# Kernel optimization log

Measured on AMD Instinct MI355X. Metric: run time of the kernel, lower is better.

Reference implementation:

```python
import jax, jax.numpy as jnp
import numpy as np

NEG_INF = -1e30  # stand-in for -inf, avoids NaN under masked rows edge cases


def setup_inputs() -> dict:
    key = jax.random.key(0)
    ks = jax.random.split(key, 6)
    H, N, F_IN, HD, F_OUT = 8, 4096, 512, 64, 512
    X = jax.random.normal(ks[0], (H, N, F_IN), dtype=jnp.float32)
    mask = jax.random.randint(ks[1], (H, N, N), 0, 2, dtype=jnp.int32)
    s = 1.0 / np.sqrt(F_IN)
    W_Q = jax.random.normal(ks[2], (H, HD, F_IN), dtype=jnp.float32) * s
    W_K = jax.random.normal(ks[3], (H, HD, F_IN), dtype=jnp.float32) * s
    W_V = jax.random.normal(ks[4], (H, HD, F_IN), dtype=jnp.float32) * s
    W_O = jax.random.normal(ks[5], (F_OUT, H * HD), dtype=jnp.float32) * (1.0 / np.sqrt(H * HD))
    return {"X": X, "mask": mask, "W_Q": W_Q, "W_K": W_K, "W_V": W_V, "W_O": W_O}


def reference(X, mask, W_Q, W_K, W_V, W_O):
    # X: [H, N, F_in]; W_{Q,K,V}: [H, head_dim, F_in] (torch Linear layout: [out,in])
    Q = jnp.einsum('hnf,hdf->hnd', X, W_Q)
    K = jnp.einsum('hnf,hdf->hnd', X, W_K)
    V = jnp.einsum('hnf,hdf->hnd', X, W_V)
    head_dim = K.shape[-1]
    E = jnp.einsum('hnd,hmd->hnm', Q, K) / jnp.sqrt(jnp.float32(head_dim))  # [H,N,N]
    E = jnp.where(mask == 0, jnp.float32(NEG_INF), E)
    A = jax.nn.softmax(E, axis=-1)
    Hout = jnp.einsum('hnm,hmd->hnd', A, V)  # [H, N, head_dim]
    # concat heads along feature dim -> [N, H*head_dim]
    Hcat = jnp.transpose(Hout, (1, 0, 2)).reshape(Hout.shape[1], -1)
    # dropout is identity in eval mode
    return Hcat @ W_O.T  # [N, fan_out]
```

## Files before the change

### kernel.cpp

```cpp
#include <hip/hip_runtime.h>

typedef __bf16 bf16x8 __attribute__((ext_vector_type(8)));
typedef float f32x4 __attribute__((ext_vector_type(4)));
typedef int i32x4 __attribute__((ext_vector_type(4)));

#define MFMA(a, b, c) __builtin_amdgcn_mfma_f32_16x16x32_bf16((a), (b), (c), 0, 0, 0)
#define GLOAD_LDS(g, l) __builtin_amdgcn_global_load_lds( \
    (const __attribute__((address_space(1))) void*)(g),   \
    (__attribute__((address_space(3))) void*)(l), 16, 0, 0)

constexpr int HEADS = 8, SEQ = 4096, FIN = 512, HD = 64, FOUT = 512;
constexpr float QSCALE = 0.18033688011112042f;

__device__ inline bf16x8 cvt8(const float* __restrict__ p) {
    f32x4 a = *(const f32x4*)p;
    f32x4 b = *(const f32x4*)(p + 4);
    bf16x8 r;
    r[0] = (__bf16)a[0]; r[1] = (__bf16)a[1]; r[2] = (__bf16)a[2]; r[3] = (__bf16)a[3];
    r[4] = (__bf16)b[0]; r[5] = (__bf16)b[1]; r[6] = (__bf16)b[2]; r[7] = (__bf16)b[3];
    return r;
}

__global__ __launch_bounds__(256) void qkv_kernel(
    const float* __restrict__ X, const float* __restrict__ Wq,
    const float* __restrict__ Wk, const float* __restrict__ Wv,
    __bf16* __restrict__ Q, __bf16* __restrict__ K, __bf16* __restrict__ Vt)
{
    const int h = blockIdx.y;
    const int tid = threadIdx.x;
    const int w = tid >> 6, lane = tid & 63;
    const int quad = lane >> 4, l16 = lane & 15;
    const int m = blockIdx.x * 64 + w * 16 + l16;

    const float* xrow = X + ((size_t)h * SEQ + m) * FIN + quad * 8;
    const float* wqh = Wq + (size_t)h * HD * FIN + quad * 8;
    const float* wkh = Wk + (size_t)h * HD * FIN + quad * 8;
    const float* wvh = Wv + (size_t)h * HD * FIN + quad * 8;

    const f32x4 vzero = {0.f, 0.f, 0.f, 0.f};
    f32x4 accQ[4], accK[4], accV[4];
#pragma unroll
    for (int t = 0; t < 4; ++t) { accQ[t] = vzero; accK[t] = vzero; accV[t] = vzero; }

    for (int f0 = 0; f0 < FIN; f0 += 32) {
        bf16x8 a = cvt8(xrow + f0);
#pragma unroll
        for (int t = 0; t < 4; ++t) {
            const int wrow = (t * 16 + l16) * FIN + f0;
            bf16x8 bq = cvt8(wqh + wrow);
            bf16x8 bk = cvt8(wkh + wrow);
            bf16x8 bv = cvt8(wvh + wrow);
            accQ[t] = MFMA(a, bq, accQ[t]);
            accK[t] = MFMA(a, bk, accK[t]);
            accV[t] = MFMA(a, bv, accV[t]);
        }
    }

    const int row0 = blockIdx.x * 64 + w * 16 + quad * 4;
#pragma unroll
    for (int t = 0; t < 4; ++t) {
        const int d = t * 16 + l16;
#pragma unroll
        for (int r = 0; r < 4; ++r) {
            const int n = row0 + r;
            Q[((size_t)h * SEQ + n) * HD + d] = (__bf16)(accQ[t][r] * QSCALE);
            K[((size_t)h * SEQ + n) * HD + d] = (__bf16)accK[t][r];
            Vt[((size_t)h * HD + d) * SEQ + n] = (__bf16)accV[t][r];
        }
    }
}

__global__ __launch_bounds__(256) void attn_kernel(
    const __bf16* __restrict__ Q, const __bf16* __restrict__ K,
    const __bf16* __restrict__ Vt, const int* __restrict__ mask,
    __bf16* __restrict__ Hcat)
{
    __shared__ __align__(16) unsigned char lds[32768 + 4 * 2048];

    const int bid = blockIdx.x;
    const int h = bid & 7;
    const int q0b = (bid >> 3) * 64;
    const int tid = threadIdx.x;
    const int w = tid >> 6, lane = tid & 63;
    const int quad = lane >> 4, l16 = lane & 15;
    const int q0 = q0b + w * 16;
    const int e7 = l16 & 7;

    __bf16* PT = (__bf16*)(lds + 32768) + w * 1024;

    const __bf16* Qh = Q + (size_t)h * SEQ * HD;
    const __bf16* Kh = K + (size_t)h * SEQ * HD;
    const __bf16* Vh = Vt + (size_t)h * HD * SEQ;
    const int* mrow = mask + ((size_t)h * SEQ + q0 + l16) * SEQ + quad * 4;

    auto stage = [&](int n0, int b) {
        unsigned char* bK = lds + b * 8192;
        unsigned char* bV = lds + 16384 + b * 8192;
#pragma unroll
        for (int c = 0; c < 2; ++c) {
            const int s = c * 256 + w * 64 + lane;
            const int row = s >> 3;
            const int cq = (s & 7) ^ (row & 7);
            GLOAD_LDS(Kh + (size_t)(n0 + row) * HD + cq * 8, bK + (c * 256 + w * 64) * 16);
            GLOAD_LDS(Vh + (size_t)row * SEQ + n0 + cq * 8, bV + (c * 256 + w * 64) * 16);
        }
    };
    auto loadM = [&](int n0, i32x4* mv) {
#pragma unroll
        for (int t = 0; t < 4; ++t) mv[t] = *(const i32x4*)(mrow + n0 + t * 16);
    };

    bf16x8 qa0 = *(const bf16x8*)(Qh + (size_t)(q0 + l16) * HD + quad * 8);
    bf16x8 qa1 = *(const bf16x8*)(Qh + (size_t)(q0 + l16) * HD + 32 + quad * 8);

    const f32x4 vzero = {0.f, 0.f, 0.f, 0.f};
    f32x4 O[4];
    float ls0 = 0.f, ls1 = 0.f, ls2 = 0.f, ls3 = 0.f;
#pragma unroll
    for (int t = 0; t < 4; ++t) O[t] = vzero;

    i32x4 mA[4], mB[4];
    stage(0, 0);
    loadM(0, mA);
    __syncthreads();

    auto tile = [&](int i, const i32x4* mc, i32x4* mn) {
        const int n0 = i * 64;
        const int cur = i & 1;
        if (i + 1 < SEQ / 64) {
            stage(n0 + 64, cur ^ 1);
            loadM(n0 + 64, mn);
        }
        const __bf16* cK = (const __bf16*)(lds + cur * 8192);
        const __bf16* cV = (const __bf16*)(lds + 16384 + cur * 8192);

        f32x4 St[4];
        __builtin_amdgcn_s_setprio(1);
#pragma unroll
        for (int t = 0; t < 4; ++t) {
            const int kr = t * 16 + l16;
            bf16x8 kb0 = *(const bf16x8*)(cK + kr * 64 + ((quad ^ (kr & 7)) * 8));
            bf16x8 kb1 = *(const bf16x8*)(cK + kr * 64 + (((quad + 4) ^ (kr & 7)) * 8));
            St[t] = MFMA(kb0, qa0, vzero);
            St[t] = MFMA(kb1, qa1, St[t]);
        }
        __builtin_amdgcn_s_setprio(0);

#pragma unroll
        for (int t = 0; t < 4; ++t) {
            union { unsigned long long u; __bf16 hh[4]; } pk;
            float psub0 = 0.f, psub1 = 0.f;
#pragma unroll
            for (int r = 0; r < 4; ++r) {
                float p = __builtin_amdgcn_exp2f(St[t][r]);
                p = mc[t][r] ? p : 0.f;
                if (r & 1) psub1 += p; else psub0 += p;
                pk.hh[r] = (__bf16)p;
            }
            if (t == 0) ls0 += psub0 + psub1;
            else if (t == 1) ls1 += psub0 + psub1;
            else if (t == 2) ls2 += psub0 + psub1;
            else ls3 += psub0 + psub1;
            const int c = t * 2 + (quad >> 1);
            *(unsigned long long*)(PT + l16 * 64 + ((c ^ e7) * 8) + (quad & 1) * 4) = pk.u;
        }

        bf16x8 pa0 = *(const bf16x8*)(PT + l16 * 64 + ((quad ^ e7) * 8));
        bf16x8 pa1 = *(const bf16x8*)(PT + l16 * 64 + (((quad + 4) ^ e7) * 8));
        __builtin_amdgcn_s_setprio(1);
#pragma unroll
        for (int t = 0; t < 4; ++t) {
            const int dr = t * 16 + l16;
            bf16x8 vb0 = *(const bf16x8*)(cV + dr * 64 + ((quad ^ (dr & 7)) * 8));
            bf16x8 vb1 = *(const bf16x8*)(cV + dr * 64 + (((quad + 4) ^ (dr & 7)) * 8));
            O[t] = MFMA(pa0, vb0, O[t]);
            O[t] = MFMA(pa1, vb1, O[t]);
        }
        __builtin_amdgcn_s_setprio(0);
        __syncthreads();
    };

    for (int i = 0; i < SEQ / 64; i += 2) {
        tile(i, mA, mB);
        tile(i + 1, mB, mA);
    }

    float lsum = (ls0 + ls1) + (ls2 + ls3);
    lsum += __shfl_xor(lsum, 16, 64);
    lsum += __shfl_xor(lsum, 32, 64);
    float inv[4];
#pragma unroll
    for (int r = 0; r < 4; ++r) {
        float Lr = __shfl(lsum, quad * 4 + r, 64);
        inv[r] = Lr > 0.f ? 1.0f / Lr : 0.f;
    }

#pragma unroll
    for (int r = 0; r < 4; ++r) {
        const int n = q0 + quad * 4 + r;
#pragma unroll
        for (int t = 0; t < 4; ++t)
            Hcat[(size_t)n * FOUT + h * HD + t * 16 + l16] = (__bf16)(O[t][r] * inv[r]);
    }
}

__global__ __launch_bounds__(256) void out_kernel(
    const __bf16* __restrict__ Hcat, const float* __restrict__ Wo,
    float* __restrict__ out)
{
    const int tid = threadIdx.x;
    const int w = tid >> 6, lane = tid & 63;
    const int quad = lane >> 4, l16 = lane & 15;
    const int n0 = blockIdx.x * 64 + w * 16;
    const int o0 = blockIdx.y * 64;

    const f32x4 vzero = {0.f, 0.f, 0.f, 0.f};
    f32x4 acc[4];
#pragma unroll
    for (int t = 0; t < 4; ++t) acc[t] = vzero;

    for (int k0 = 0; k0 < FOUT; k0 += 32) {
        bf16x8 a = *(const bf16x8*)(Hcat + (size_t)(n0 + l16) * FOUT + k0 + quad * 8);
#pragma unroll
        for (int t = 0; t < 4; ++t) {
            bf16x8 b = cvt8(Wo + (size_t)(o0 + t * 16 + l16) * FOUT + k0 + quad * 8);
            acc[t] = MFMA(a, b, acc[t]);
        }
    }
#pragma unroll
    for (int t = 0; t < 4; ++t)
#pragma unroll
        for (int r = 0; r < 4; ++r)
            out[(size_t)(n0 + quad * 4 + r) * FOUT + o0 + t * 16 + l16] = acc[t][r];
}

extern "C" void kernel_launch(void* const* d_in, const int* in_sizes, int n_in,
                              void* d_out, int out_size, void* d_ws, size_t ws_size,
                              hipStream_t stream) {
    const float* X    = (const float*)d_in[0];
    const int*   mask = (const int*)d_in[1];
    const float* Wq   = (const float*)d_in[2];
    const float* Wk   = (const float*)d_in[3];
    const float* Wv   = (const float*)d_in[4];
    const float* Wo   = (const float*)d_in[5];
    float* out = (float*)d_out;

    __bf16* Q    = (__bf16*)d_ws;
    __bf16* K    = Q + (size_t)HEADS * SEQ * HD;
    __bf16* Vt   = K + (size_t)HEADS * SEQ * HD;
    __bf16* Hcat = Vt + (size_t)HEADS * HD * SEQ;

    qkv_kernel<<<dim3(SEQ / 64, HEADS), 256, 0, stream>>>(X, Wq, Wk, Wv, Q, K, Vt);
    attn_kernel<<<(SEQ / 64) * HEADS, 256, 0, stream>>>(Q, K, Vt, mask, Hcat);
    out_kernel<<<dim3(SEQ / 64, FOUT / 64), 256, 0, stream>>>(Hcat, Wo, out);
}
```

Measured before the change: 889.5 us.

## Pack int32 mask into 64-bit bitmasks in a pre-pass before attention

Adds a pack kernel that reads the int32 attention mask once and writes one 64-bit ballot word per 64 keys per query row. The attention kernel then loads a single u64 per tile instead of four i32x4 vectors and tests bits, which cuts mask traffic and register use inside the main loop. The cost is an extra launch that still streams the full 512MB mask, plus a small workspace region for the packed words. Since the mask must be read in full either way, any gain depends on the attention loop having been limited by mask loads.

```diff
diff --git a/kernel.cpp b/kernel.cpp
--- a/kernel.cpp
+++ b/kernel.cpp
@@ -21,6 +21,20 @@
     return r;
 }
 
+__global__ __launch_bounds__(256) void pack_kernel(
+    const int* __restrict__ mask, unsigned long long* __restrict__ pmask)
+{
+    const int w = threadIdx.x >> 6, lane = threadIdx.x & 63;
+    const size_t row = (size_t)blockIdx.x * 4 + w;
+    const int* mr = mask + row * SEQ;
+    unsigned long long* pr = pmask + row * (SEQ / 64);
+    for (int tw = 0; tw < SEQ / 64; ++tw) {
+        int m = mr[tw * 64 + lane];
+        unsigned long long b = __ballot(m != 0);
+        if (lane == 0) pr[tw] = b;
+    }
+}
+
 __global__ __launch_bounds__(256) void qkv_kernel(
     const float* __restrict__ X, const float* __restrict__ Wq,
     const float* __restrict__ Wk, const float* __restrict__ Wv,
@@ -72,7 +86,7 @@
 
 __global__ __launch_bounds__(256) void attn_kernel(
     const __bf16* __restrict__ Q, const __bf16* __restrict__ K,
-    const __bf16* __restrict__ Vt, const int* __restrict__ mask,
+    const __bf16* __restrict__ Vt, const unsigned long long* __restrict__ pmask,
     __bf16* __restrict__ Hcat)
 {
     __shared__ __align__(16) unsigned char lds[32768 + 4 * 2048];
@@ -85,13 +99,14 @@
     const int quad = lane >> 4, l16 = lane & 15;
     const int q0 = q0b + w * 16;
     const int e7 = l16 & 7;
+    const int qsh = quad * 4;
 
     __bf16* PT = (__bf16*)(lds + 32768) + w * 1024;
 
     const __bf16* Qh = Q + (size_t)h * SEQ * HD;
     const __bf16* Kh = K + (size_t)h * SEQ * HD;
     const __bf16* Vh = Vt + (size_t)h * HD * SEQ;
-    const int* mrow = mask + ((size_t)h * SEQ + q0 + l16) * SEQ + quad * 4;
+    const unsigned long long* pmr = pmask + ((size_t)h * SEQ + q0 + l16) * (SEQ / 64);
 
     auto stage = [&](int n0, int b) {
         unsigned char* bK = lds + b * 8192;
@@ -105,10 +120,6 @@
             GLOAD_LDS(Vh + (size_t)row * SEQ + n0 + cq * 8, bV + (c * 256 + w * 64) * 16);
         }
     };
-    auto loadM = [&](int n0, i32x4* mv) {
-#pragma unroll
-        for (int t = 0; t < 4; ++t) mv[t] = *(const i32x4*)(mrow + n0 + t * 16);
-    };
 
     bf16x8 qa0 = *(const bf16x8*)(Qh + (size_t)(q0 + l16) * HD + quad * 8);
     bf16x8 qa1 = *(const bf16x8*)(Qh + (size_t)(q0 + l16) * HD + 32 + quad * 8);
@@ -119,17 +130,17 @@
 #pragma unroll
     for (int t = 0; t < 4; ++t) O[t] = vzero;
 
-    i32x4 mA[4], mB[4];
+    unsigned long long mA, mB;
     stage(0, 0);
-    loadM(0, mA);
+    mA = pmr[0];
     __syncthreads();
 
-    auto tile = [&](int i, const i32x4* mc, i32x4* mn) {
+    auto tile = [&](int i, unsigned long long mc, unsigned long long* mn) {
         const int n0 = i * 64;
         const int cur = i & 1;
         if (i + 1 < SEQ / 64) {
             stage(n0 + 64, cur ^ 1);
-            loadM(n0 + 64, mn);
+            *mn = pmr[i + 1];
         }
         const __bf16* cK = (const __bf16*)(lds + cur * 8192);
         const __bf16* cV = (const __bf16*)(lds + 16384 + cur * 8192);
@@ -146,14 +157,16 @@
         }
         __builtin_amdgcn_s_setprio(0);
 
-#pragma unroll
-        for (int t = 0; t < 4; ++t) {
+        const unsigned mlo = (unsigned)mc, mhi = (unsigned)(mc >> 32);
+#pragma unroll
+        for (int t = 0; t < 4; ++t) {
+            const unsigned ms = (((t & 2) ? mhi : mlo) >> ((t & 1) * 16)) >> qsh;
             union { unsigned long long u; __bf16 hh[4]; } pk;
             float psub0 = 0.f, psub1 = 0.f;
 #pragma unroll
             for (int r = 0; r < 4; ++r) {
                 float p = __builtin_amdgcn_exp2f(St[t][r]);
-                p = mc[t][r] ? p : 0.f;
+                p = (ms & (1u << r)) ? p : 0.f;
                 if (r & 1) psub1 += p; else psub0 += p;
                 pk.hh[r] = (__bf16)p;
             }
@@ -181,8 +194,8 @@
     };
 
     for (int i = 0; i < SEQ / 64; i += 2) {
-        tile(i, mA, mB);
-        tile(i + 1, mB, mA);
+        tile(i, mA, &mB);
+        tile(i + 1, mB, &mA);
     }
 
     float lsum = (ls0 + ls1) + (ls2 + ls3);
@@ -249,8 +262,10 @@
     __bf16* K    = Q + (size_t)HEADS * SEQ * HD;
     __bf16* Vt   = K + (size_t)HEADS * SEQ * HD;
     __bf16* Hcat = Vt + (size_t)HEADS * HD * SEQ;
-
+    unsigned long long* pmask = (unsigned long long*)(Hcat + (size_t)SEQ * FOUT);
+
+    pack_kernel<<<HEADS * SEQ / 4, 256, 0, stream>>>(mask, pmask);
     qkv_kernel<<<dim3(SEQ / 64, HEADS), 256, 0, stream>>>(X, Wq, Wk, Wv, Q, K, Vt);
-    attn_kernel<<<(SEQ / 64) * HEADS, 256, 0, stream>>>(Q, K, Vt, mask, Hcat);
+    attn_kernel<<<(SEQ / 64) * HEADS, 256, 0, stream>>>(Q, K, Vt, pmask, Hcat);
     out_kernel<<<dim3(SEQ / 64, FOUT / 64), 256, 0, stream>>>(Hcat, Wo, out);
 }
```

After: 976.5 us. 1.1x slower.

## Load K and V tiles directly from global memory instead of LDS staging

Applied to the files above, without the earlier changes.

Removes the double-buffered global_load_lds staging of K and V tiles and the per-tile block barrier. Each wave now reads its K and V fragments straight from global memory, relying on L1/L2 caching since all four waves of a block read the same tiles. This frees LDS, which could raise occupancy, and removes the synchronisation. The cost is redundant global loads per wave and no explicit prefetch, so load latency now sits directly in front of the MFMAs.

```diff
diff --git a/kernel.cpp b/kernel.cpp
--- a/kernel.cpp
+++ b/kernel.cpp
@@ -5,9 +5,6 @@
 typedef int i32x4 __attribute__((ext_vector_type(4)));
 
 #define MFMA(a, b, c) __builtin_amdgcn_mfma_f32_16x16x32_bf16((a), (b), (c), 0, 0, 0)
-#define GLOAD_LDS(g, l) __builtin_amdgcn_global_load_lds( \
-    (const __attribute__((address_space(1))) void*)(g),   \
-    (__attribute__((address_space(3))) void*)(l), 16, 0, 0)
 
 constexpr int HEADS = 8, SEQ = 4096, FIN = 512, HD = 64, FOUT = 512;
 constexpr float QSCALE = 0.18033688011112042f;
@@ -75,7 +72,7 @@
     const __bf16* __restrict__ Vt, const int* __restrict__ mask,
     __bf16* __restrict__ Hcat)
 {
-    __shared__ __align__(16) unsigned char lds[32768 + 4 * 2048];
+    __shared__ __align__(16) __bf16 PT_lds[4 * 1024];
 
     const int bid = blockIdx.x;
     const int h = bid & 7;
@@ -86,25 +83,13 @@
     const int q0 = q0b + w * 16;
     const int e7 = l16 & 7;
 
-    __bf16* PT = (__bf16*)(lds + 32768) + w * 1024;
+    __bf16* PT = PT_lds + w * 1024;
 
     const __bf16* Qh = Q + (size_t)h * SEQ * HD;
     const __bf16* Kh = K + (size_t)h * SEQ * HD;
     const __bf16* Vh = Vt + (size_t)h * HD * SEQ;
     const int* mrow = mask + ((size_t)h * SEQ + q0 + l16) * SEQ + quad * 4;
 
-    auto stage = [&](int n0, int b) {
-        unsigned char* bK = lds + b * 8192;
-        unsigned char* bV = lds + 16384 + b * 8192;
-#pragma unroll
-        for (int c = 0; c < 2; ++c) {
-            const int s = c * 256 + w * 64 + lane;
-            const int row = s >> 3;
-            const int cq = (s & 7) ^ (row & 7);
-            GLOAD_LDS(Kh + (size_t)(n0 + row) * HD + cq * 8, bK + (c * 256 + w * 64) * 16);
-            GLOAD_LDS(Vh + (size_t)row * SEQ + n0 + cq * 8, bV + (c * 256 + w * 64) * 16);
-        }
-    };
     auto loadM = [&](int n0, i32x4* mv) {
 #pragma unroll
         for (int t = 0; t < 4; ++t) mv[t] = *(const i32x4*)(mrow + n0 + t * 16);
@@ -120,27 +105,19 @@
     for (int t = 0; t < 4; ++t) O[t] = vzero;
 
     i32x4 mA[4], mB[4];
-    stage(0, 0);
     loadM(0, mA);
-    __syncthreads();
 
     auto tile = [&](int i, const i32x4* mc, i32x4* mn) {
         const int n0 = i * 64;
-        const int cur = i & 1;
-        if (i + 1 < SEQ / 64) {
-            stage(n0 + 64, cur ^ 1);
-            loadM(n0 + 64, mn);
-        }
-        const __bf16* cK = (const __bf16*)(lds + cur * 8192);
-        const __bf16* cV = (const __bf16*)(lds + 16384 + cur * 8192);
+        if (i + 1 < SEQ / 64) loadM(n0 + 64, mn);
 
         f32x4 St[4];
         __builtin_amdgcn_s_setprio(1);
 #pragma unroll
         for (int t = 0; t < 4; ++t) {
-            const int kr = t * 16 + l16;
-            bf16x8 kb0 = *(const bf16x8*)(cK + kr * 64 + ((quad ^ (kr & 7)) * 8));
-            bf16x8 kb1 = *(const bf16x8*)(cK + kr * 64 + (((quad + 4) ^ (kr & 7)) * 8));
+            const __bf16* krow = Kh + (size_t)(n0 + t * 16 + l16) * HD;
+            bf16x8 kb0 = *(const bf16x8*)(krow + quad * 8);
+            bf16x8 kb1 = *(const bf16x8*)(krow + 32 + quad * 8);
             St[t] = MFMA(kb0, qa0, vzero);
             St[t] = MFMA(kb1, qa1, St[t]);
         }
@@ -170,14 +147,13 @@
         __builtin_amdgcn_s_setprio(1);
 #pragma unroll
         for (int t = 0; t < 4; ++t) {
-            const int dr = t * 16 + l16;
-            bf16x8 vb0 = *(const bf16x8*)(cV + dr * 64 + ((quad ^ (dr & 7)) * 8));
-            bf16x8 vb1 = *(const bf16x8*)(cV + dr * 64 + (((quad + 4) ^ (dr & 7)) * 8));
+            const __bf16* vrow = Vh + (size_t)(t * 16 + l16) * SEQ + n0;
+            bf16x8 vb0 = *(const bf16x8*)(vrow + quad * 8);
+            bf16x8 vb1 = *(const bf16x8*)(vrow + 32 + quad * 8);
             O[t] = MFMA(pa0, vb0, O[t]);
             O[t] = MFMA(pa1, vb1, O[t]);
         }
         __builtin_amdgcn_s_setprio(0);
-        __syncthreads();
     };
 
     for (int i = 0; i < SEQ / 64; i += 2) {
```

New measurement: 1.036 ms. 16.4% more time.

## Use 32x32 MFMA with split-K warps in attention and pre-convert weights to bf16

Applied to the files above, without the earlier changes.

The attention kernel now uses 32x32x16 MFMAs. Each wave handles 32 queries and half of each 64-key tile, and the P operand is rebuilt through cross-lane shuffles instead of an LDS round trip. The two key-halves' partial outputs and row sums are reduced through LDS at the end, and stores are vectorized. A separate kernel converts the weight matrices to bf16 once per call, so the projection kernels load bf16 directly instead of converting fp32 in their inner loops. This adds a launch and a final LDS reduction, and the attention loop remains bound by streaming the int32 mask.

```diff
diff --git a/kernel.cpp b/kernel.cpp
--- a/kernel.cpp
+++ b/kernel.cpp
@@ -2,9 +2,11 @@
 
 typedef __bf16 bf16x8 __attribute__((ext_vector_type(8)));
 typedef float f32x4 __attribute__((ext_vector_type(4)));
+typedef float f32x16 __attribute__((ext_vector_type(16)));
 typedef int i32x4 __attribute__((ext_vector_type(4)));
 
-#define MFMA(a, b, c) __builtin_amdgcn_mfma_f32_16x16x32_bf16((a), (b), (c), 0, 0, 0)
+#define MFMA16(a, b, c) __builtin_amdgcn_mfma_f32_16x16x32_bf16((a), (b), (c), 0, 0, 0)
+#define MFMA32(a, b, c) __builtin_amdgcn_mfma_f32_32x32x16_bf16((a), (b), (c), 0, 0, 0)
 #define GLOAD_LDS(g, l) __builtin_amdgcn_global_load_lds( \
     (const __attribute__((address_space(1))) void*)(g),   \
     (__attribute__((address_space(3))) void*)(l), 16, 0, 0)
@@ -21,9 +23,28 @@
     return r;
 }
 
+__device__ inline unsigned pack2(float a, float b) {
+    union { unsigned u; __bf16 h[2]; } r;
+    r.h[0] = (__bf16)a; r.h[1] = (__bf16)b;
+    return r.u;
+}
+
+__global__ __launch_bounds__(256) void wconv_kernel(
+    const float* __restrict__ Wq, const float* __restrict__ Wk,
+    const float* __restrict__ Wv, const float* __restrict__ Wo,
+    __bf16* __restrict__ oq, __bf16* __restrict__ ok,
+    __bf16* __restrict__ ov, __bf16* __restrict__ oo)
+{
+    const int which = blockIdx.y;
+    const float* s = which == 0 ? Wq : which == 1 ? Wk : which == 2 ? Wv : Wo;
+    __bf16* d = which == 0 ? oq : which == 1 ? ok : which == 2 ? ov : oo;
+    const size_t i = ((size_t)blockIdx.x * 256 + threadIdx.x) * 8;
+    *(bf16x8*)(d + i) = cvt8(s + i);
+}
+
 __global__ __launch_bounds__(256) void qkv_kernel(
-    const float* __restrict__ X, const float* __restrict__ Wq,
-    const float* __restrict__ Wk, const float* __restrict__ Wv,
+    const float* __restrict__ X, const __bf16* __restrict__ Wq,
+    const __bf16* __restrict__ Wk, const __bf16* __restrict__ Wv,
     __bf16* __restrict__ Q, __bf16* __restrict__ K, __bf16* __restrict__ Vt)
 {
     const int h = blockIdx.y;
@@ -33,9 +54,9 @@
     const int m = blockIdx.x * 64 + w * 16 + l16;
 
     const float* xrow = X + ((size_t)h * SEQ + m) * FIN + quad * 8;
-    const float* wqh = Wq + (size_t)h * HD * FIN + quad * 8;
-    const float* wkh = Wk + (size_t)h * HD * FIN + quad * 8;
-    const float* wvh = Wv + (size_t)h * HD * FIN + quad * 8;
+    const __bf16* wqh = Wq + (size_t)h * HD * FIN + quad * 8;
+    const __bf16* wkh = Wk + (size_t)h * HD * FIN + quad * 8;
+    const __bf16* wvh = Wv + (size_t)h * HD * FIN + quad * 8;
 
     const f32x4 vzero = {0.f, 0.f, 0.f, 0.f};
     f32x4 accQ[4], accK[4], accV[4];
@@ -47,12 +68,12 @@
 #pragma unroll
         for (int t = 0; t < 4; ++t) {
             const int wrow = (t * 16 + l16) * FIN + f0;
-            bf16x8 bq = cvt8(wqh + wrow);
-            bf16x8 bk = cvt8(wkh + wrow);
-            bf16x8 bv = cvt8(wvh + wrow);
-            accQ[t] = MFMA(a, bq, accQ[t]);
-            accK[t] = MFMA(a, bk, accK[t]);
-            accV[t] = MFMA(a, bv, accV[t]);
+            bf16x8 bq = *(const bf16x8*)(wqh + wrow);
+            bf16x8 bk = *(const bf16x8*)(wkh + wrow);
+            bf16x8 bv = *(const bf16x8*)(wvh + wrow);
+            accQ[t] = MFMA16(a, bq, accQ[t]);
+            accK[t] = MFMA16(a, bk, accK[t]);
+            accV[t] = MFMA16(a, bv, accV[t]);
         }
     }
 
@@ -75,23 +96,22 @@
     const __bf16* __restrict__ Vt, const int* __restrict__ mask,
     __bf16* __restrict__ Hcat)
 {
-    __shared__ __align__(16) unsigned char lds[32768 + 4 * 2048];
+    __shared__ __align__(16) unsigned char lds[4 * 32 * 68 * 4 + 4 * 32 * 4];
 
     const int bid = blockIdx.x;
     const int h = bid & 7;
     const int q0b = (bid >> 3) * 64;
     const int tid = threadIdx.x;
     const int w = tid >> 6, lane = tid & 63;
-    const int quad = lane >> 4, l16 = lane & 15;
-    const int q0 = q0b + w * 16;
-    const int e7 = l16 & 7;
-
-    __bf16* PT = (__bf16*)(lds + 32768) + w * 1024;
+    const int qh = w >> 1;
+    const int kh = w & 1;
+    const int l32 = lane & 31;
+    const int hi = lane >> 5;
 
     const __bf16* Qh = Q + (size_t)h * SEQ * HD;
     const __bf16* Kh = K + (size_t)h * SEQ * HD;
     const __bf16* Vh = Vt + (size_t)h * HD * SEQ;
-    const int* mrow = mask + ((size_t)h * SEQ + q0 + l16) * SEQ + quad * 4;
+    const int* mrow = mask + ((size_t)h * SEQ + q0b + qh * 32 + l32) * SEQ + kh * 32 + hi * 4;
 
     auto stage = [&](int n0, int b) {
         unsigned char* bK = lds + b * 8192;
@@ -107,22 +127,24 @@
     };
     auto loadM = [&](int n0, i32x4* mv) {
 #pragma unroll
-        for (int t = 0; t < 4; ++t) mv[t] = *(const i32x4*)(mrow + n0 + t * 16);
+        for (int c = 0; c < 4; ++c) mv[c] = *(const i32x4*)(mrow + n0 + c * 8);
     };
 
-    bf16x8 qa0 = *(const bf16x8*)(Qh + (size_t)(q0 + l16) * HD + quad * 8);
-    bf16x8 qa1 = *(const bf16x8*)(Qh + (size_t)(q0 + l16) * HD + 32 + quad * 8);
-
-    const f32x4 vzero = {0.f, 0.f, 0.f, 0.f};
-    f32x4 O[4];
+    bf16x8 qb[4];
+#pragma unroll
+    for (int s = 0; s < 4; ++s)
+        qb[s] = *(const bf16x8*)(Qh + (size_t)(q0b + qh * 32 + l32) * HD + s * 16 + hi * 8);
+
+    f32x16 O0 = {}, O1 = {};
     float ls0 = 0.f, ls1 = 0.f, ls2 = 0.f, ls3 = 0.f;
-#pragma unroll
-    for (int t = 0; t < 4; ++t) O[t] = vzero;
 
     i32x4 mA[4], mB[4];
     stage(0, 0);
     loadM(0, mA);
     __syncthreads();
+
+    const int krow = kh * 32 + l32;
+    const int ksw = krow & 7;
 
     auto tile = [&](int i, const i32x4* mc, i32x4* mn) {
         const int n0 = i * 64;
@@ -134,47 +156,59 @@
         const __bf16* cK = (const __bf16*)(lds + cur * 8192);
         const __bf16* cV = (const __bf16*)(lds + 16384 + cur * 8192);
 
-        f32x4 St[4];
+        f32x16 St = {};
         __builtin_amdgcn_s_setprio(1);
 #pragma unroll
-        for (int t = 0; t < 4; ++t) {
-            const int kr = t * 16 + l16;
-            bf16x8 kb0 = *(const bf16x8*)(cK + kr * 64 + ((quad ^ (kr & 7)) * 8));
-            bf16x8 kb1 = *(const bf16x8*)(cK + kr * 64 + (((quad + 4) ^ (kr & 7)) * 8));
-            St[t] = MFMA(kb0, qa0, vzero);
-            St[t] = MFMA(kb1, qa1, St[t]);
+        for (int s = 0; s < 4; ++s) {
+            bf16x8 ka = *(const bf16x8*)(cK + krow * 64 + (((2 * s + hi) ^ ksw) * 8));
+            St = MFMA32(ka, qb[s], St);
         }
         __builtin_amdgcn_s_setprio(0);
 
-#pragma unroll
-        for (int t = 0; t < 4; ++t) {
-            union { unsigned long long u; __bf16 hh[4]; } pk;
-            float psub0 = 0.f, psub1 = 0.f;
-#pragma unroll
-            for (int r = 0; r < 4; ++r) {
-                float p = __builtin_amdgcn_exp2f(St[t][r]);
-                p = mc[t][r] ? p : 0.f;
-                if (r & 1) psub1 += p; else psub0 += p;
-                pk.hh[r] = (__bf16)p;
+        float p[16];
+#pragma unroll
+        for (int c = 0; c < 4; ++c) {
+            float a0 = 0.f, a1 = 0.f;
+#pragma unroll
+            for (int j = 0; j < 4; ++j) {
+                float e = __builtin_amdgcn_exp2f(St[c * 4 + j]);
+                e = mc[c][j] ? e : 0.f;
+                if (j & 1) a1 += e; else a0 += e;
+                p[c * 4 + j] = e;
             }
-            if (t == 0) ls0 += psub0 + psub1;
-            else if (t == 1) ls1 += psub0 + psub1;
-            else if (t == 2) ls2 += psub0 + psub1;
-            else ls3 += psub0 + psub1;
-            const int c = t * 2 + (quad >> 1);
-            *(unsigned long long*)(PT + l16 * 64 + ((c ^ e7) * 8) + (quad & 1) * 4) = pk.u;
-        }
-
-        bf16x8 pa0 = *(const bf16x8*)(PT + l16 * 64 + ((quad ^ e7) * 8));
-        bf16x8 pa1 = *(const bf16x8*)(PT + l16 * 64 + (((quad + 4) ^ e7) * 8));
+            if (c == 0) ls0 += a0 + a1;
+            else if (c == 1) ls1 += a0 + a1;
+            else if (c == 2) ls2 += a0 + a1;
+            else ls3 += a0 + a1;
+        }
+
+        bf16x8 pa[2];
+#pragma unroll
+        for (int sp = 0; sp < 2; ++sp) {
+            unsigned u0 = pack2(p[sp * 8 + 0], p[sp * 8 + 1]);
+            unsigned u1 = pack2(p[sp * 8 + 2], p[sp * 8 + 3]);
+            unsigned u2 = pack2(p[sp * 8 + 4], p[sp * 8 + 5]);
+            unsigned u3 = pack2(p[sp * 8 + 6], p[sp * 8 + 7]);
+            unsigned s0 = (unsigned)__shfl_xor((int)u0, 32, 64);
+            unsigned s1 = (unsigned)__shfl_xor((int)u1, 32, 64);
+            unsigned s2 = (unsigned)__shfl_xor((int)u2, 32, 64);
+            unsigned s3 = (unsigned)__shfl_xor((int)u3, 32, 64);
+            union { unsigned u[4]; bf16x8 v; } A;
+            A.u[0] = hi ? s2 : u0;
+            A.u[1] = hi ? s3 : u1;
+            A.u[2] = hi ? u2 : s0;
+            A.u[3] = hi ? u3 : s1;
+            pa[sp] = A.v;
+        }
+
         __builtin_amdgcn_s_setprio(1);
 #pragma unroll
-        for (int t = 0; t < 4; ++t) {
-            const int dr = t * 16 + l16;
-            bf16x8 vb0 = *(const bf16x8*)(cV + dr * 64 + ((quad ^ (dr & 7)) * 8));
-            bf16x8 vb1 = *(const bf16x8*)(cV + dr * 64 + (((quad + 4) ^ (dr & 7)) * 8));
-            O[t] = MFMA(pa0, vb0, O[t]);
-            O[t] = MFMA(pa1, vb1, O[t]);
+        for (int sp = 0; sp < 2; ++sp) {
+            const int g = kh * 4 + 2 * sp + hi;
+            bf16x8 vb0 = *(const bf16x8*)(cV + l32 * 64 + ((g ^ (l32 & 7)) * 8));
+            bf16x8 vb1 = *(const bf16x8*)(cV + (32 + l32) * 64 + ((g ^ ((32 + l32) & 7)) * 8));
+            O0 = MFMA32(pa[sp], vb0, O0);
+            O1 = MFMA32(pa[sp], vb1, O1);
         }
         __builtin_amdgcn_s_setprio(0);
         __syncthreads();
@@ -185,27 +219,45 @@
         tile(i + 1, mB, mA);
     }
 
+    float* Of = (float*)lds;
+    float* Lf = (float*)lds + 4 * 32 * 68;
     float lsum = (ls0 + ls1) + (ls2 + ls3);
-    lsum += __shfl_xor(lsum, 16, 64);
     lsum += __shfl_xor(lsum, 32, 64);
-    float inv[4];
-#pragma unroll
-    for (int r = 0; r < 4; ++r) {
-        float Lr = __shfl(lsum, quad * 4 + r, 64);
-        inv[r] = Lr > 0.f ? 1.0f / Lr : 0.f;
-    }
-
-#pragma unroll
-    for (int r = 0; r < 4; ++r) {
-        const int n = q0 + quad * 4 + r;
-#pragma unroll
-        for (int t = 0; t < 4; ++t)
-            Hcat[(size_t)n * FOUT + h * HD + t * 16 + l16] = (__bf16)(O[t][r] * inv[r]);
-    }
+    float* myO = Of + w * (32 * 68);
+#pragma unroll
+    for (int r = 0; r < 16; ++r) {
+        const int qr = (r & 3) + 8 * (r >> 2) + 4 * hi;
+        myO[qr * 68 + l32] = O0[r];
+        myO[qr * 68 + 32 + l32] = O1[r];
+    }
+    if (lane < 32) Lf[w * 32 + lane] = lsum;
+    __syncthreads();
+
+    const int q = tid >> 2, hd0 = (tid & 3) * 16;
+    const int qg = q >> 5, q32 = q & 31;
+    const float l = Lf[qg * 64 + q32] + Lf[qg * 64 + 32 + q32];
+    const float inv = l > 0.f ? 1.0f / l : 0.f;
+    float acc[16];
+#pragma unroll
+    for (int v = 0; v < 4; ++v) {
+        f32x4 a = *(const f32x4*)(Of + (2 * qg) * (32 * 68) + q32 * 68 + hd0 + v * 4);
+        f32x4 b = *(const f32x4*)(Of + (2 * qg + 1) * (32 * 68) + q32 * 68 + hd0 + v * 4);
+#pragma unroll
+        for (int j = 0; j < 4; ++j) acc[v * 4 + j] = a[j] + b[j];
+    }
+    bf16x8 o0, o1;
+#pragma unroll
+    for (int j = 0; j < 8; ++j) {
+        o0[j] = (__bf16)(acc[j] * inv);
+        o1[j] = (__bf16)(acc[8 + j] * inv);
+    }
+    __bf16* dst = Hcat + (size_t)(q0b + q) * FOUT + h * HD + hd0;
+    *(bf16x8*)dst = o0;
+    *(bf16x8*)(dst + 8) = o1;
 }
 
 __global__ __launch_bounds__(256) void out_kernel(
-    const __bf16* __restrict__ Hcat, const float* __restrict__ Wo,
+    const __bf16* __restrict__ Hcat, const __bf16* __restrict__ Wo,
     float* __restrict__ out)
 {
     const int tid = threadIdx.x;
@@ -223,8 +275,8 @@
         bf16x8 a = *(const bf16x8*)(Hcat + (size_t)(n0 + l16) * FOUT + k0 + quad * 8);
 #pragma unroll
         for (int t = 0; t < 4; ++t) {
-            bf16x8 b = cvt8(Wo + (size_t)(o0 + t * 16 + l16) * FOUT + k0 + quad * 8);
-            acc[t] = MFMA(a, b, acc[t]);
+            bf16x8 b = *(const bf16x8*)(Wo + (size_t)(o0 + t * 16 + l16) * FOUT + k0 + quad * 8);
+            acc[t] = MFMA16(a, b, acc[t]);
         }
     }
 #pragma unroll
@@ -249,8 +301,13 @@
     __bf16* K    = Q + (size_t)HEADS * SEQ * HD;
     __bf16* Vt   = K + (size_t)HEADS * SEQ * HD;
     __bf16* Hcat = Vt + (size_t)HEADS * HD * SEQ;
-
-    qkv_kernel<<<dim3(SEQ / 64, HEADS), 256, 0, stream>>>(X, Wq, Wk, Wv, Q, K, Vt);
+    __bf16* Wqb  = Hcat + (size_t)SEQ * FOUT;
+    __bf16* Wkb  = Wqb + (size_t)HEADS * HD * FIN;
+    __bf16* Wvb  = Wkb + (size_t)HEADS * HD * FIN;
+    __bf16* Wob  = Wvb + (size_t)HEADS * HD * FIN;
+
+    wconv_kernel<<<dim3(128, 4), 256, 0, stream>>>(Wq, Wk, Wv, Wo, Wqb, Wkb, Wvb, Wob);
+    qkv_kernel<<<dim3(SEQ / 64, HEADS), 256, 0, stream>>>(X, Wqb, Wkb, Wvb, Q, K, Vt);
     attn_kernel<<<(SEQ / 64) * HEADS, 256, 0, stream>>>(Q, K, Vt, mask, Hcat);
-    out_kernel<<<dim3(SEQ / 64, FOUT / 64), 256, 0, stream>>>(Hcat, Wo, out);
-}
+    out_kernel<<<dim3(SEQ / 64, FOUT / 64), 256, 0, stream>>>(Hcat, Wob, out);
+}
```

Measured after the change: 821.9 us. 1.08x faster.
